# Kernel tuning notes

Hardware: AMD Instinct MI355X
Metric: run time of the kernel (lower is better)

## Reference

```python
import jax, jax.numpy as jnp
import numpy as np

EPS = jnp.finfo(jnp.float32).eps


def setup_inputs() -> dict:
    key = jax.random.key(0)
    k0, k1, k2 = jax.random.split(key, 3)
    B, N = 1, 4194304
    cloud_t0 = jax.random.normal(k0, (B, N, 3), dtype=jnp.float32)
    cloud_t1 = jax.random.normal(k1, (B, N, 3), dtype=jnp.float32)
    weights = jax.random.uniform(k2, (B, N), dtype=jnp.float32)
    return {"cloud_t0": cloud_t0, "cloud_t1": cloud_t1, "weights": weights}


def reference(cloud_t0, cloud_t1, weights):
    # use_epsilon_on_weights = False branch
    count_nonzero = jnp.sum(weights > 0.0, axis=-1)
    not_enough_points = count_nonzero < 3
    weights = weights + (not_enough_points.astype(weights.dtype) * EPS)[:, None]

    cum_wts = jnp.sum(weights, axis=-1)                      # (B,)
    w = weights[:, :, None]                                   # (B,N,1)
    mx = jnp.sum(cloud_t0 * w, axis=1) / cum_wts[:, None]     # (B,3) weighted centroid
    my = jnp.sum(cloud_t1 * w, axis=1) / cum_wts[:, None]
    Xc = cloud_t0 - mx[:, None, :]
    Yc = cloud_t1 - my[:, None, :]
    # weighted cross-covariance: (B,3,3)
    Sxy = jnp.einsum('bno,bni->boi', Yc * w, Xc) / cum_wts[:, None, None]

    U, D, Vh = jnp.linalg.svd(Sxy, full_matrices=False)       # torch.svd returns V = Vh^T
    V = jnp.swapaxes(Vh, -1, -2)

    # rank via torch.linalg.matrix_rank default tol: max_sv * max(m,n) * eps
    tol = D.max(axis=-1) * 3 * EPS
    rank = jnp.sum(D > tol[:, None], axis=-1)

    det_S = jnp.linalg.det(Sxy)
    det_mul = jnp.linalg.det(U) * jnp.linalg.det(V)
    sign_full = jnp.where(det_S < 0.0, -1.0, 1.0)             # rank == 3 case
    sign_def = jnp.where(jnp.isclose(det_mul, -1.0), -1.0, 1.0)  # rank == 2 case
    s = jnp.where(rank > 2, sign_full, sign_def)              # (B,)

    # R = U @ diag(1,1,s) @ V^T
    diag = jnp.stack([jnp.ones_like(s), jnp.ones_like(s), s], axis=-1)  # (B,3)
    R = jnp.einsum('boc,bc,bic->boi', U, diag, V)             # (B,3,3)
    t = my - jnp.einsum('boc,bc->bo', R, mx)                  # (B,3)

    B = R.shape[0]
    R4 = jnp.concatenate([R, jnp.zeros((B, 1, 3), R.dtype)], axis=1)    # (B,4,3)
    t4 = jnp.concatenate([t, jnp.ones((B, 1), t.dtype)], axis=-1)       # (B,4)
    T = jnp.concatenate([R4, t4[:, :, None]], axis=-1)        # (B,4,4)
    return T, not_enough_points
```

## Files before the change

### kernel.cpp

```cpp
#include <hip/hip_runtime.h>
#include <math.h>

#define NACC 32
#define TILE 1024

__device__ __forceinline__ void accum_point(float w, float x0, float x1, float x2,
                                            float y0, float y1, float y2, float* a) {
    a[0] += (w > 0.0f) ? 1.0f : 0.0f;
    a[1] += w;
    a[2] = fmaf(w, x0, a[2]); a[3] = fmaf(w, x1, a[3]); a[4] = fmaf(w, x2, a[4]);
    float wy0 = w * y0, wy1 = w * y1, wy2 = w * y2;
    a[5] += wy0; a[6] += wy1; a[7] += wy2;
    a[8]  = fmaf(wy0, x0, a[8]);  a[9]  = fmaf(wy0, x1, a[9]);  a[10] = fmaf(wy0, x2, a[10]);
    a[11] = fmaf(wy1, x0, a[11]); a[12] = fmaf(wy1, x1, a[12]); a[13] = fmaf(wy1, x2, a[13]);
    a[14] = fmaf(wy2, x0, a[14]); a[15] = fmaf(wy2, x1, a[15]); a[16] = fmaf(wy2, x2, a[16]);
    a[17] += x0; a[18] += x1; a[19] += x2;
    a[20] += y0; a[21] += y1; a[22] += y2;
    a[23] = fmaf(y0, x0, a[23]); a[24] = fmaf(y0, x1, a[24]); a[25] = fmaf(y0, x2, a[25]);
    a[26] = fmaf(y1, x0, a[26]); a[27] = fmaf(y1, x1, a[27]); a[28] = fmaf(y1, x2, a[28]);
    a[29] = fmaf(y2, x0, a[29]); a[30] = fmaf(y2, x1, a[30]); a[31] = fmaf(y2, x2, a[31]);
}

__global__ __launch_bounds__(256) void kabsch_reduce(
    const float* __restrict__ c0, const float* __restrict__ c1,
    const float* __restrict__ w, int N, float* __restrict__ partials, int nblocks) {
    __shared__ float4 sA[TILE];
    __shared__ float4 sB[TILE];
    __shared__ float  sw[TILE];
    __shared__ float  wred[4][NACC];

    float a[NACC];
    #pragma unroll
    for (int i = 0; i < NACC; ++i) a[i] = 0.0f;

    const int t = threadIdx.x;
    const int lane = t & 63, wave = t >> 6;
    const float4* A4 = (const float4*)c0;
    const float4* B4 = (const float4*)c1;
    const float4* W4 = (const float4*)w;
    float* fA = (float*)sA;
    float* fB = (float*)sB;

    int nfull = N >> 10;

    for (int tile = blockIdx.x; tile < nfull; tile += gridDim.x) {
        int baseAB = tile * 768;
        #pragma unroll
        for (int k = 0; k < 3; ++k) {
            int idx = (k << 8) + t;
            float4 va = A4[baseAB + idx];
            float4 vb = B4[baseAB + idx];
            unsigned flat0 = (unsigned)idx << 2;
            float aa[4] = { va.x, va.y, va.z, va.w };
            float bb[4] = { vb.x, vb.y, vb.z, vb.w };
            #pragma unroll
            for (int j = 0; j < 4; ++j) {
                unsigned f = flat0 + j;
                unsigned p = (f * 21846u) >> 16;
                unsigned cc = f - p * 3u;
                fA[(p << 2) | cc] = aa[j];
                fB[(p << 2) | cc] = bb[j];
            }
        }
        ((float4*)sw)[t] = W4[(tile << 8) + t];
        __syncthreads();
        #pragma unroll
        for (int k = 0; k < 4; ++k) {
            int p = t + (k << 8);
            float4 xa = sA[p];
            float4 xb = sB[p];
            float wt = sw[p];
            accum_point(wt, xa.x, xa.y, xa.z, xb.x, xb.y, xb.z, a);
        }
        __syncthreads();
    }
    if (blockIdx.x == 0 && t == 0) {
        for (int i = nfull << 10; i < N; ++i)
            accum_point(w[i], c0[3*i], c0[3*i+1], c0[3*i+2],
                        c1[3*i], c1[3*i+1], c1[3*i+2], a);
    }

    {
        int hi;
        hi = lane & 1;
        #pragma unroll
        for (int i = 0; i < 16; ++i) {
            float send = hi ? a[i] : a[i + 16];
            float recv = __shfl_xor(send, 1, 64);
            a[i] = (hi ? a[i + 16] : a[i]) + recv;
        }
        hi = lane & 2;
        #pragma unroll
        for (int i = 0; i < 8; ++i) {
            float send = hi ? a[i] : a[i + 8];
            float recv = __shfl_xor(send, 2, 64);
            a[i] = (hi ? a[i + 8] : a[i]) + recv;
        }
        hi = lane & 4;
        #pragma unroll
        for (int i = 0; i < 4; ++i) {
            float send = hi ? a[i] : a[i + 4];
            float recv = __shfl_xor(send, 4, 64);
            a[i] = (hi ? a[i + 4] : a[i]) + recv;
        }
        hi = lane & 8;
        #pragma unroll
        for (int i = 0; i < 2; ++i) {
            float send = hi ? a[i] : a[i + 2];
            float recv = __shfl_xor(send, 8, 64);
            a[i] = (hi ? a[i + 2] : a[i]) + recv;
        }
        hi = lane & 16;
        {
            float send = hi ? a[0] : a[1];
            float recv = __shfl_xor(send, 16, 64);
            a[0] = (hi ? a[1] : a[0]) + recv;
        }
        a[0] += __shfl_xor(a[0], 32, 64);
    }
    if (lane < 32) {
        int acc = ((lane & 1) << 4) | ((lane & 2) << 2) | (lane & 4)
                | ((lane & 8) >> 2) | ((lane & 16) >> 4);
        wred[wave][acc] = a[0];
    }
    __syncthreads();
    if (t < NACC)
        partials[t * nblocks + blockIdx.x] =
            wred[0][t] + wred[1][t] + wred[2][t] + wred[3][t];
}

__device__ __forceinline__ double det3(const double m[3][3]) {
    return m[0][0] * (m[1][1] * m[2][2] - m[1][2] * m[2][1])
         - m[0][1] * (m[1][0] * m[2][2] - m[1][2] * m[2][0])
         + m[0][2] * (m[1][0] * m[2][1] - m[1][1] * m[2][0]);
}

__global__ __launch_bounds__(256) void kabsch_finalize(
    const float* __restrict__ partials, int nblocks, int N, float* __restrict__ out) {
    double d[NACC];
    #pragma unroll
    for (int i = 0; i < NACC; ++i) d[i] = 0.0;
    for (int m = threadIdx.x; m < nblocks; m += 256) {
        #pragma unroll
        for (int i = 0; i < NACC; ++i)
            d[i] += (double)partials[i * nblocks + m];
    }
    #pragma unroll
    for (int off = 32; off > 0; off >>= 1) {
        #pragma unroll
        for (int i = 0; i < NACC; ++i) d[i] += __shfl_down(d[i], off, 64);
    }
    __shared__ double sm[4][NACC];
    int wave = threadIdx.x >> 6, lane = threadIdx.x & 63;
    if (lane == 0) {
        #pragma unroll
        for (int i = 0; i < NACC; ++i) sm[wave][i] = d[i];
    }
    __syncthreads();
    if (threadIdx.x != 0) return;
    #pragma unroll
    for (int i = 0; i < NACC; ++i) d[i] = sm[0][i] + sm[1][i] + sm[2][i] + sm[3][i];

    const double EPSF = (double)1.1920929e-7f;
    double cnt = d[0];
    double W = d[1];
    double swx[3] = { d[2], d[3], d[4] };
    double swy[3] = { d[5], d[6], d[7] };
    double swyx[9];
    for (int i = 0; i < 9; ++i) swyx[i] = d[8 + i];
    bool nep = cnt < 3.0;
    if (nep) {
        W += EPSF * (double)N;
        for (int i = 0; i < 3; ++i) { swx[i] += EPSF * d[17 + i]; swy[i] += EPSF * d[20 + i]; }
        for (int i = 0; i < 9; ++i) swyx[i] += EPSF * d[23 + i];
    }

    double mx[3], my[3];
    for (int i = 0; i < 3; ++i) { mx[i] = swx[i] / W; my[i] = swy[i] / W; }
    double S[3][3];
    for (int o = 0; o < 3; ++o)
        for (int i = 0; i < 3; ++i)
            S[o][i] = swyx[o * 3 + i] / W - my[o] * mx[i];

    double Bm[3][3], V[3][3];
    for (int i = 0; i < 3; ++i)
        for (int j = 0; j < 3; ++j) {
            double acc = 0.0;
            for (int k = 0; k < 3; ++k) acc += S[k][i] * S[k][j];
            Bm[i][j] = acc;
            V[i][j] = (i == j) ? 1.0 : 0.0;
        }
    for (int sweep = 0; sweep < 30; ++sweep) {
        double off2 = Bm[0][1]*Bm[0][1] + Bm[0][2]*Bm[0][2] + Bm[1][2]*Bm[1][2];
        double diag2 = Bm[0][0]*Bm[0][0] + Bm[1][1]*Bm[1][1] + Bm[2][2]*Bm[2][2];
        if (off2 <= diag2 * 1e-32 + 1e-300) break;
        for (int pair = 0; pair < 3; ++pair) {
            int p = (pair == 2) ? 1 : 0;
            int q = (pair == 0) ? 1 : 2;
            double apq = Bm[p][q];
            if (fabs(apq) < 1e-300) continue;
            double theta = (Bm[q][q] - Bm[p][p]) / (2.0 * apq);
            double tt = ((theta >= 0.0) ? 1.0 : -1.0) / (fabs(theta) + sqrt(1.0 + theta * theta));
            double c = 1.0 / sqrt(1.0 + tt * tt);
            double sn = tt * c;
            for (int k = 0; k < 3; ++k) {
                double bkp = Bm[k][p], bkq = Bm[k][q];
                Bm[k][p] = c * bkp - sn * bkq;
                Bm[k][q] = sn * bkp + c * bkq;
            }
            for (int k = 0; k < 3; ++k) {
                double bpk = Bm[p][k], bqk = Bm[q][k];
                Bm[p][k] = c * bpk - sn * bqk;
                Bm[q][k] = sn * bpk + c * bqk;
            }
            for (int k = 0; k < 3; ++k) {
                double vkp = V[k][p], vkq = V[k][q];
                V[k][p] = c * vkp - sn * vkq;
                V[k][q] = sn * vkp + c * vkq;
            }
        }
    }
    double lam[3] = { Bm[0][0], Bm[1][1], Bm[2][2] };
    for (int i = 0; i < 2; ++i)
        for (int j = i + 1; j < 3; ++j)
            if (lam[j] > lam[i]) {
                double tl = lam[i]; lam[i] = lam[j]; lam[j] = tl;
                for (int k = 0; k < 3; ++k) { double tv = V[k][i]; V[k][i] = V[k][j]; V[k][j] = tv; }
            }
    double sig[3];
    for (int i = 0; i < 3; ++i) sig[i] = sqrt(fmax(lam[i], 0.0));

    double U[3][3];
    for (int i = 0; i < 3; ++i) {
        double u0 = S[0][0]*V[0][i] + S[0][1]*V[1][i] + S[0][2]*V[2][i];
        double u1 = S[1][0]*V[0][i] + S[1][1]*V[1][i] + S[1][2]*V[2][i];
        double u2 = S[2][0]*V[0][i] + S[2][1]*V[1][i] + S[2][2]*V[2][i];
        double nrm = sqrt(u0*u0 + u1*u1 + u2*u2);
        if (nrm > 1e-150) {
            U[0][i] = u0 / nrm; U[1][i] = u1 / nrm; U[2][i] = u2 / nrm;
        } else if (i == 0) {
            U[0][0] = 1.0; U[1][0] = 0.0; U[2][0] = 0.0;
        } else if (i == 1) {
            double e0 = (fabs(U[0][0]) < 0.9) ? 1.0 : 0.0;
            double e1 = 1.0 - e0;
            double dp = e0 * U[0][0] + e1 * U[1][0];
            double v0 = e0 - dp * U[0][0], v1 = e1 - dp * U[1][0], v2 = -dp * U[2][0];
            double n2 = sqrt(v0*v0 + v1*v1 + v2*v2);
            U[0][1] = v0 / n2; U[1][1] = v1 / n2; U[2][1] = v2 / n2;
        } else {
            U[0][2] = U[1][0]*U[2][1] - U[2][0]*U[1][1];
            U[1][2] = U[2][0]*U[0][1] - U[0][0]*U[2][1];
            U[2][2] = U[0][0]*U[1][1] - U[1][0]*U[0][1];
        }
    }

    double tol = sig[0] * 3.0 * EPSF;
    int rank = (sig[0] > tol) + (sig[1] > tol) + (sig[2] > tol);
    double detS = det3(S);
    double det_mul = det3(U) * det3(V);
    double sign_full = (detS < 0.0) ? -1.0 : 1.0;
    double sign_def = (fabs(det_mul + 1.0) <= 1.00001e-5) ? -1.0 : 1.0;
    double s = (rank > 2) ? sign_full : sign_def;

    double R[3][3];
    for (int o = 0; o < 3; ++o)
        for (int i = 0; i < 3; ++i)
            R[o][i] = U[o][0]*V[i][0] + U[o][1]*V[i][1] + s * U[o][2]*V[i][2];
    double tv[3];
    for (int o = 0; o < 3; ++o)
        tv[o] = my[o] - (R[o][0]*mx[0] + R[o][1]*mx[1] + R[o][2]*mx[2]);

    for (int o = 0; o < 3; ++o) {
        out[o * 4 + 0] = (float)R[o][0];
        out[o * 4 + 1] = (float)R[o][1];
        out[o * 4 + 2] = (float)R[o][2];
        out[o * 4 + 3] = (float)tv[o];
    }
    out[12] = 0.0f; out[13] = 0.0f; out[14] = 0.0f; out[15] = 1.0f;
    out[16] = nep ? 1.0f : 0.0f;
}

extern "C" void kernel_launch(void* const* d_in, const int* in_sizes, int n_in,
                              void* d_out, int out_size, void* d_ws, size_t ws_size,
                              hipStream_t stream) {
    const float* c0 = (const float*)d_in[0];
    const float* c1 = (const float*)d_in[1];
    const float* w  = (const float*)d_in[2];
    float* out = (float*)d_out;
    int N = in_sizes[2];

    int blocks = 1024;
    size_t need = (size_t)blocks * NACC * sizeof(float);
    if (need > ws_size) {
        blocks = (int)(ws_size / (NACC * sizeof(float)));
        if (blocks < 1) blocks = 1;
    }
    float* partials = (float*)d_ws;

    kabsch_reduce<<<blocks, 256, 0, stream>>>(c0, c1, w, N, partials, blocks);
    kabsch_finalize<<<1, 256, 0, stream>>>(partials, blocks, N, out);
}
```

Baseline: 152.4 us.

## Load four points per thread directly from global, drop LDS staging

Replaces the shared-memory transpose tile, with its two barriers per tile, by a grid-stride loop in which each thread loads three float4 from each cloud plus one float4 of weights and processes four whole points. This removes the LDS traffic, index arithmetic and syncs. In exchange, per-thread global loads are strided by 48 bytes across lanes rather than fully contiguous, which may reduce coalescing efficiency, and register pressure rises.

Result: no change. 152.4 us (-0.0%).

```diff
diff --git a/kernel.cpp b/kernel.cpp
--- a/kernel.cpp
+++ b/kernel.cpp
@@ -2,7 +2,6 @@
 #include <math.h>
 
 #define NACC 32
-#define TILE 1024
 
 __device__ __forceinline__ void accum_point(float w, float x0, float x1, float x2,
                                             float y0, float y1, float y2, float* a) {
@@ -24,10 +23,7 @@
 __global__ __launch_bounds__(256) void kabsch_reduce(
     const float* __restrict__ c0, const float* __restrict__ c1,
     const float* __restrict__ w, int N, float* __restrict__ partials, int nblocks) {
-    __shared__ float4 sA[TILE];
-    __shared__ float4 sB[TILE];
-    __shared__ float  sw[TILE];
-    __shared__ float  wred[4][NACC];
+    __shared__ float wred[4][NACC];
 
     float a[NACC];
     #pragma unroll
@@ -35,47 +31,24 @@
 
     const int t = threadIdx.x;
     const int lane = t & 63, wave = t >> 6;
-    const float4* A4 = (const float4*)c0;
-    const float4* B4 = (const float4*)c1;
-    const float4* W4 = (const float4*)w;
-    float* fA = (float*)sA;
-    float* fB = (float*)sB;
-
-    int nfull = N >> 10;
-
-    for (int tile = blockIdx.x; tile < nfull; tile += gridDim.x) {
-        int baseAB = tile * 768;
-        #pragma unroll
-        for (int k = 0; k < 3; ++k) {
-            int idx = (k << 8) + t;
-            float4 va = A4[baseAB + idx];
-            float4 vb = B4[baseAB + idx];
-            unsigned flat0 = (unsigned)idx << 2;
-            float aa[4] = { va.x, va.y, va.z, va.w };
-            float bb[4] = { vb.x, vb.y, vb.z, vb.w };
-            #pragma unroll
-            for (int j = 0; j < 4; ++j) {
-                unsigned f = flat0 + j;
-                unsigned p = (f * 21846u) >> 16;
-                unsigned cc = f - p * 3u;
-                fA[(p << 2) | cc] = aa[j];
-                fB[(p << 2) | cc] = bb[j];
-            }
-        }
-        ((float4*)sw)[t] = W4[(tile << 8) + t];
-        __syncthreads();
-        #pragma unroll
-        for (int k = 0; k < 4; ++k) {
-            int p = t + (k << 8);
-            float4 xa = sA[p];
-            float4 xb = sB[p];
-            float wt = sw[p];
-            accum_point(wt, xa.x, xa.y, xa.z, xb.x, xb.y, xb.z, a);
-        }
-        __syncthreads();
+    const float4* __restrict__ A4 = (const float4*)c0;
+    const float4* __restrict__ B4 = (const float4*)c1;
+    const float4* __restrict__ W4 = (const float4*)w;
+
+    const int ngrp = N >> 2;
+    const int stride = gridDim.x << 8;
+    for (int g = (blockIdx.x << 8) + t; g < ngrp; g += stride) {
+        int i3 = 3 * g;
+        float4 a0 = A4[i3], a1 = A4[i3 + 1], a2 = A4[i3 + 2];
+        float4 b0 = B4[i3], b1 = B4[i3 + 1], b2 = B4[i3 + 2];
+        float4 vw = W4[g];
+        accum_point(vw.x, a0.x, a0.y, a0.z, b0.x, b0.y, b0.z, a);
+        accum_point(vw.y, a0.w, a1.x, a1.y, b0.w, b1.x, b1.y, a);
+        accum_point(vw.z, a1.z, a1.w, a2.x, b1.z, b1.w, b2.x, a);
+        accum_point(vw.w, a2.y, a2.z, a2.w, b2.y, b2.z, b2.w, a);
     }
     if (blockIdx.x == 0 && t == 0) {
-        for (int i = nfull << 10; i < N; ++i)
+        for (int i = (N >> 2) << 2; i < N; ++i)
             accum_point(w[i], c0[3*i], c0[3*i+1], c0[3*i+2],
                         c1[3*i], c1[3*i+1], c1[3*i+2], a);
     }
```
